# Performance work log

Hardware: AMD Instinct MI355X
Metric: run time of the kernel (lower is better)

## Reference

```python
import jax, jax.numpy as jnp
import numpy as np

EPS = 1e-5
CH = 8            # channels_per_head
HID = 4           # max(CH // reduction, 4)
SCALE = CH ** -0.5


def _layernorm(x, g, b):
    mu = jnp.mean(x, axis=-1, keepdims=True)
    var = jnp.mean(jnp.square(x - mu), axis=-1, keepdims=True)
    return (x - mu) * jax.lax.rsqrt(var + EPS) * g + b


def setup_inputs() -> dict:
    key = jax.random.key(0)
    ks = jax.random.split(key, 12)
    s = 1.0 / np.sqrt(CH)
    sh = 1.0 / np.sqrt(HID)
    return {
        "x": jax.random.normal(ks[0], (32, 4, CH, 256, 256), dtype=jnp.float32),
        "Wq": jax.random.uniform(ks[1], (CH, CH), jnp.float32, -s, s),
        "Wk": jax.random.uniform(ks[2], (CH, CH), jnp.float32, -s, s),
        "Wv": jax.random.uniform(ks[3], (CH, CH), jnp.float32, -s, s),
        "Wo": jax.random.uniform(ks[4], (CH, CH), jnp.float32, -s, s),
        "bo": jax.random.uniform(ks[5], (CH,), jnp.float32, -s, s),
        "W1": jax.random.uniform(ks[6], (HID, CH), jnp.float32, -s, s),
        "b1": jax.random.uniform(ks[7], (HID,), jnp.float32, -s, s),
        "W2": jax.random.uniform(ks[8], (CH, HID), jnp.float32, -sh, sh),
        "b2": jax.random.uniform(ks[9], (CH,), jnp.float32, -sh, sh),
        "g1": jnp.ones((CH,), jnp.float32),
        "beta1": jnp.zeros((CH,), jnp.float32),
        "g2": jnp.ones((CH,), jnp.float32),
        "beta2": jnp.zeros((CH,), jnp.float32),
        "gate": jnp.full((1,), 0.5, jnp.float32),
    }


def reference(x, Wq, Wk, Wv, Wo, bo, W1, b1, W2, b2, g1, beta1, g2, beta2, gate):
    # x: (B, n_heads, CH, H, W); pool over spatial dims -> (B, n_heads, CH)
    x_pooled = jnp.mean(x, axis=(-2, -1))
    xn = _layernorm(x_pooled, g1, beta1)
    Q = xn @ Wq.T
    K = xn @ Wk.T
    V = xn @ Wv.T
    # tiny attention across heads: scores (B, n_heads, n_heads)
    attn = jax.nn.softmax(jnp.einsum('bhc,bgc->bhg', Q, K) * SCALE, axis=-1)
    attn_out = jnp.einsum('bhg,bgc->bhc', attn, V) @ Wo.T + bo
    x_attn = x_pooled + attn_out
    xn2 = _layernorm(x_attn, g2, beta2)
    ffn = jax.nn.gelu(xn2 @ W1.T + b1, approximate=False) @ W2.T + b2
    x_out = x_attn + ffn
    g = jax.nn.sigmoid(gate)
    aw = g * (x_out - x_pooled) + x_pooled      # (B, n_heads, CH)
    return x * (1.0 + aw[..., None, None])
```

## Files before the change

### kernel.cpp

```cpp
#include <hip/hip_runtime.h>
#include <math.h>

#define CH 8
#define NH 4
#define HID 4
#define SPATIAL 65536
#define NSLICE 1024
#define NHALF  2048
#define HALF4  8192
#define EPS 1e-5f

typedef float nf4 __attribute__((ext_vector_type(4)));

__global__ __launch_bounds__(256)
void pool_kernel(const float* __restrict__ x, float* __restrict__ partial) {
    const int half = blockIdx.x;
    const nf4* xs = (const nf4*)x + (size_t)half * HALF4;
    const int tid = threadIdx.x;

    nf4 a0 = {0,0,0,0}, a1 = {0,0,0,0}, a2 = {0,0,0,0}, a3 = {0,0,0,0};
    int k = tid;
#pragma unroll
    for (int it = 0; it < 8; ++it) {
        a0 += xs[k];
        a1 += xs[k + 256];
        a2 += xs[k + 512];
        a3 += xs[k + 768];
        k += 1024;
    }
    nf4 a = (a0 + a1) + (a2 + a3);
    float sum = (a.x + a.y) + (a.z + a.w);

    for (int off = 32; off; off >>= 1) sum += __shfl_down(sum, off, 64);
    __shared__ float part[4];
    if ((tid & 63) == 0) part[tid >> 6] = sum;
    __syncthreads();
    if (tid == 0)
        partial[half] = (part[0] + part[1]) + (part[2] + part[3]);
}

__global__ __launch_bounds__(256)
void scale_fused(const float* __restrict__ x,
                 const float* __restrict__ partial,
                 const float* __restrict__ Wq, const float* __restrict__ Wk,
                 const float* __restrict__ Wv, const float* __restrict__ Wo,
                 const float* __restrict__ bo,
                 const float* __restrict__ W1, const float* __restrict__ b1,
                 const float* __restrict__ W2, const float* __restrict__ b2,
                 const float* __restrict__ g1, const float* __restrict__ beta1,
                 const float* __restrict__ g2, const float* __restrict__ beta2,
                 const float* __restrict__ gate,
                 float* __restrict__ out) {
    const int half  = blockIdx.x;
    const int slice = half >> 1;
    const int b     = slice >> 5;
    const int hh    = (slice >> 3) & 3;
    const int cc    = slice & 7;
    const int tid   = threadIdx.x;

    __shared__ float Kl[NH][CH], Vl[NH][CH], fac[NH][CH];

    float xp[CH], Q[CH];
    if (tid < NH) {
        const float* pr = partial + b * (NH * CH * 2) + tid * (CH * 2);
#pragma unroll
        for (int c = 0; c < CH; ++c)
            xp[c] = (pr[c * 2] + pr[c * 2 + 1]) * (1.0f / SPATIAL);
        float mu = 0.f;
#pragma unroll
        for (int c = 0; c < CH; ++c) mu += xp[c];
        mu *= 0.125f;
        float var = 0.f;
#pragma unroll
        for (int c = 0; c < CH; ++c) { float d = xp[c] - mu; var += d * d; }
        var *= 0.125f;
        float rs = rsqrtf(var + EPS);
        float xn[CH];
#pragma unroll
        for (int c = 0; c < CH; ++c) xn[c] = (xp[c] - mu) * rs * g1[c] + beta1[c];
#pragma unroll
        for (int c = 0; c < CH; ++c) {
            float q = 0.f, k = 0.f, v = 0.f;
#pragma unroll
            for (int j = 0; j < CH; ++j) {
                q += xn[j] * Wq[c * CH + j];
                k += xn[j] * Wk[c * CH + j];
                v += xn[j] * Wv[c * CH + j];
            }
            Q[c] = q; Kl[tid][c] = k; Vl[tid][c] = v;
        }
    }
    __syncthreads();
    if (tid < NH) {
        float sc[NH], mx = -1e30f;
#pragma unroll
        for (int g = 0; g < NH; ++g) {
            float s = 0.f;
#pragma unroll
            for (int c = 0; c < CH; ++c) s += Q[c] * Kl[g][c];
            s *= 0.35355339059327373f;
            sc[g] = s; mx = fmaxf(mx, s);
        }
        float den = 0.f;
#pragma unroll
        for (int g = 0; g < NH; ++g) { sc[g] = __expf(sc[g] - mx); den += sc[g]; }
        const float inv = 1.0f / den;
        float ao[CH];
#pragma unroll
        for (int c = 0; c < CH; ++c) {
            float a = 0.f;
#pragma unroll
            for (int g = 0; g < NH; ++g) a += sc[g] * Vl[g][c];
            ao[c] = a * inv;
        }
        float xa[CH];
#pragma unroll
        for (int c = 0; c < CH; ++c) {
            float o = bo[c];
#pragma unroll
            for (int j = 0; j < CH; ++j) o += ao[j] * Wo[c * CH + j];
            xa[c] = xp[c] + o;
        }
        float mu = 0.f;
#pragma unroll
        for (int c = 0; c < CH; ++c) mu += xa[c];
        mu *= 0.125f;
        float var = 0.f;
#pragma unroll
        for (int c = 0; c < CH; ++c) { float d = xa[c] - mu; var += d * d; }
        var *= 0.125f;
        float rs = rsqrtf(var + EPS);
        float xn2[CH];
#pragma unroll
        for (int c = 0; c < CH; ++c) xn2[c] = (xa[c] - mu) * rs * g2[c] + beta2[c];
        float h1[HID];
#pragma unroll
        for (int i = 0; i < HID; ++i) {
            float t = b1[i];
#pragma unroll
            for (int c = 0; c < CH; ++c) t += xn2[c] * W1[i * CH + c];
            h1[i] = 0.5f * t * (1.0f + erff(t * 0.70710678118654752f));
        }
        const float gs = 1.0f / (1.0f + __expf(-gate[0]));
#pragma unroll
        for (int c = 0; c < CH; ++c) {
            float f = b2[c];
#pragma unroll
            for (int i = 0; i < HID; ++i) f += h1[i] * W2[c * HID + i];
            float xo = xa[c] + f;
            fac[tid][c] = 1.0f + gs * (xo - xp[c]) + xp[c];
        }
    }
    __syncthreads();
    const float f = fac[hh][cc];

    const nf4* xs = (const nf4*)x + (size_t)half * HALF4;
    nf4*       os = (nf4*)out     + (size_t)half * HALF4;
    int k = tid;
#pragma unroll
    for (int it = 0; it < 8; ++it) {
        nf4 v0 = xs[k];
        nf4 v1 = xs[k + 256];
        nf4 v2 = xs[k + 512];
        nf4 v3 = xs[k + 768];
        v0 *= f; v1 *= f; v2 *= f; v3 *= f;
        __builtin_nontemporal_store(v0, &os[k]);
        __builtin_nontemporal_store(v1, &os[k + 256]);
        __builtin_nontemporal_store(v2, &os[k + 512]);
        __builtin_nontemporal_store(v3, &os[k + 768]);
        k += 1024;
    }
}

extern "C" void kernel_launch(void* const* d_in, const int* in_sizes, int n_in,
                              void* d_out, int out_size, void* d_ws, size_t ws_size,
                              hipStream_t stream) {
    const float* x     = (const float*)d_in[0];
    const float* Wq    = (const float*)d_in[1];
    const float* Wk    = (const float*)d_in[2];
    const float* Wv    = (const float*)d_in[3];
    const float* Wo    = (const float*)d_in[4];
    const float* bo    = (const float*)d_in[5];
    const float* W1    = (const float*)d_in[6];
    const float* b1    = (const float*)d_in[7];
    const float* W2    = (const float*)d_in[8];
    const float* b2    = (const float*)d_in[9];
    const float* g1    = (const float*)d_in[10];
    const float* beta1 = (const float*)d_in[11];
    const float* g2    = (const float*)d_in[12];
    const float* beta2 = (const float*)d_in[13];
    const float* gate  = (const float*)d_in[14];
    float* out = (float*)d_out;

    float* partial = (float*)d_ws;

    pool_kernel<<<NHALF, 256, 0, stream>>>(x, partial);
    scale_fused<<<NHALF, 256, 0, stream>>>(x, partial,
                                           Wq, Wk, Wv, Wo, bo,
                                           W1, b1, W2, b2,
                                           g1, beta1, g2, beta2,
                                           gate, out);
}
```

Measured before the change: 129.7 us.

## Fuse pooling and scaling into one cooperative kernel with grid sync

Replaces the separate pooling and scaling kernels with a single persistent cooperative kernel. Each block pools its slices, then a grid-wide barrier precedes recomputation of the tiny attention/FFN and the scaling pass. This is meant to remove the second launch and the inter-kernel gap. In exchange it adds the grid-sync cost and ties the grid size to occupancy queries.

```diff
diff --git a/kernel.cpp b/kernel.cpp
--- a/kernel.cpp
+++ b/kernel.cpp
@@ -1,5 +1,8 @@
 #include <hip/hip_runtime.h>
+#include <hip/hip_cooperative_groups.h>
 #include <math.h>
+
+namespace cg = cooperative_groups;
 
 #define CH 8
 #define NH 4
@@ -12,163 +15,170 @@
 
 typedef float nf4 __attribute__((ext_vector_type(4)));
 
-__global__ __launch_bounds__(256)
-void pool_kernel(const float* __restrict__ x, float* __restrict__ partial) {
-    const int half = blockIdx.x;
-    const nf4* xs = (const nf4*)x + (size_t)half * HALF4;
+__global__ __launch_bounds__(256, 8)
+void fused_all(const float* __restrict__ x,
+               const float* __restrict__ Wq, const float* __restrict__ Wk,
+               const float* __restrict__ Wv, const float* __restrict__ Wo,
+               const float* __restrict__ bo,
+               const float* __restrict__ W1, const float* __restrict__ b1,
+               const float* __restrict__ W2, const float* __restrict__ b2,
+               const float* __restrict__ g1, const float* __restrict__ beta1,
+               const float* __restrict__ g2, const float* __restrict__ beta2,
+               const float* __restrict__ gate,
+               float* __restrict__ out,
+               float* __restrict__ partial,
+               int hpb) {
     const int tid = threadIdx.x;
-
-    nf4 a0 = {0,0,0,0}, a1 = {0,0,0,0}, a2 = {0,0,0,0}, a3 = {0,0,0,0};
-    int k = tid;
-#pragma unroll
-    for (int it = 0; it < 8; ++it) {
-        a0 += xs[k];
-        a1 += xs[k + 256];
-        a2 += xs[k + 512];
-        a3 += xs[k + 768];
-        k += 1024;
+    const int h0  = blockIdx.x * hpb;
+
+    __shared__ float part[4];
+    __shared__ float Kl[NH][CH], Vl[NH][CH], fac[NH][CH];
+
+    for (int i = 0; i < hpb; ++i) {
+        const int half = h0 + i;
+        if (half >= NHALF) break;
+        const nf4* xs = (const nf4*)x + (size_t)half * HALF4;
+        nf4 a0 = {0,0,0,0}, a1 = {0,0,0,0}, a2 = {0,0,0,0}, a3 = {0,0,0,0};
+        int k = tid;
+#pragma unroll
+        for (int it = 0; it < 8; ++it) {
+            a0 += xs[k];
+            a1 += xs[k + 256];
+            a2 += xs[k + 512];
+            a3 += xs[k + 768];
+            k += 1024;
+        }
+        nf4 a = (a0 + a1) + (a2 + a3);
+        float sum = (a.x + a.y) + (a.z + a.w);
+        for (int off = 32; off; off >>= 1) sum += __shfl_down(sum, off, 64);
+        if ((tid & 63) == 0) part[tid >> 6] = sum;
+        __syncthreads();
+        if (tid == 0)
+            partial[half] = (part[0] + part[1]) + (part[2] + part[3]);
+        __syncthreads();
     }
-    nf4 a = (a0 + a1) + (a2 + a3);
-    float sum = (a.x + a.y) + (a.z + a.w);
-
-    for (int off = 32; off; off >>= 1) sum += __shfl_down(sum, off, 64);
-    __shared__ float part[4];
-    if ((tid & 63) == 0) part[tid >> 6] = sum;
-    __syncthreads();
-    if (tid == 0)
-        partial[half] = (part[0] + part[1]) + (part[2] + part[3]);
-}
-
-__global__ __launch_bounds__(256)
-void scale_fused(const float* __restrict__ x,
-                 const float* __restrict__ partial,
-                 const float* __restrict__ Wq, const float* __restrict__ Wk,
-                 const float* __restrict__ Wv, const float* __restrict__ Wo,
-                 const float* __restrict__ bo,
-                 const float* __restrict__ W1, const float* __restrict__ b1,
-                 const float* __restrict__ W2, const float* __restrict__ b2,
-                 const float* __restrict__ g1, const float* __restrict__ beta1,
-                 const float* __restrict__ g2, const float* __restrict__ beta2,
-                 const float* __restrict__ gate,
-                 float* __restrict__ out) {
-    const int half  = blockIdx.x;
-    const int slice = half >> 1;
-    const int b     = slice >> 5;
-    const int hh    = (slice >> 3) & 3;
-    const int cc    = slice & 7;
-    const int tid   = threadIdx.x;
-
-    __shared__ float Kl[NH][CH], Vl[NH][CH], fac[NH][CH];
-
-    float xp[CH], Q[CH];
-    if (tid < NH) {
-        const float* pr = partial + b * (NH * CH * 2) + tid * (CH * 2);
-#pragma unroll
-        for (int c = 0; c < CH; ++c)
-            xp[c] = (pr[c * 2] + pr[c * 2 + 1]) * (1.0f / SPATIAL);
-        float mu = 0.f;
-#pragma unroll
-        for (int c = 0; c < CH; ++c) mu += xp[c];
-        mu *= 0.125f;
-        float var = 0.f;
-#pragma unroll
-        for (int c = 0; c < CH; ++c) { float d = xp[c] - mu; var += d * d; }
-        var *= 0.125f;
-        float rs = rsqrtf(var + EPS);
-        float xn[CH];
-#pragma unroll
-        for (int c = 0; c < CH; ++c) xn[c] = (xp[c] - mu) * rs * g1[c] + beta1[c];
-#pragma unroll
-        for (int c = 0; c < CH; ++c) {
-            float q = 0.f, k = 0.f, v = 0.f;
-#pragma unroll
-            for (int j = 0; j < CH; ++j) {
-                q += xn[j] * Wq[c * CH + j];
-                k += xn[j] * Wk[c * CH + j];
-                v += xn[j] * Wv[c * CH + j];
-            }
-            Q[c] = q; Kl[tid][c] = k; Vl[tid][c] = v;
-        }
-    }
-    __syncthreads();
-    if (tid < NH) {
-        float sc[NH], mx = -1e30f;
-#pragma unroll
-        for (int g = 0; g < NH; ++g) {
-            float s = 0.f;
-#pragma unroll
-            for (int c = 0; c < CH; ++c) s += Q[c] * Kl[g][c];
-            s *= 0.35355339059327373f;
-            sc[g] = s; mx = fmaxf(mx, s);
-        }
-        float den = 0.f;
-#pragma unroll
-        for (int g = 0; g < NH; ++g) { sc[g] = __expf(sc[g] - mx); den += sc[g]; }
-        const float inv = 1.0f / den;
-        float ao[CH];
-#pragma unroll
-        for (int c = 0; c < CH; ++c) {
-            float a = 0.f;
-#pragma unroll
-            for (int g = 0; g < NH; ++g) a += sc[g] * Vl[g][c];
-            ao[c] = a * inv;
-        }
-        float xa[CH];
-#pragma unroll
-        for (int c = 0; c < CH; ++c) {
-            float o = bo[c];
-#pragma unroll
-            for (int j = 0; j < CH; ++j) o += ao[j] * Wo[c * CH + j];
-            xa[c] = xp[c] + o;
-        }
-        float mu = 0.f;
-#pragma unroll
-        for (int c = 0; c < CH; ++c) mu += xa[c];
-        mu *= 0.125f;
-        float var = 0.f;
-#pragma unroll
-        for (int c = 0; c < CH; ++c) { float d = xa[c] - mu; var += d * d; }
-        var *= 0.125f;
-        float rs = rsqrtf(var + EPS);
-        float xn2[CH];
-#pragma unroll
-        for (int c = 0; c < CH; ++c) xn2[c] = (xa[c] - mu) * rs * g2[c] + beta2[c];
-        float h1[HID];
-#pragma unroll
-        for (int i = 0; i < HID; ++i) {
-            float t = b1[i];
-#pragma unroll
-            for (int c = 0; c < CH; ++c) t += xn2[c] * W1[i * CH + c];
-            h1[i] = 0.5f * t * (1.0f + erff(t * 0.70710678118654752f));
-        }
-        const float gs = 1.0f / (1.0f + __expf(-gate[0]));
-#pragma unroll
-        for (int c = 0; c < CH; ++c) {
-            float f = b2[c];
-#pragma unroll
-            for (int i = 0; i < HID; ++i) f += h1[i] * W2[c * HID + i];
-            float xo = xa[c] + f;
-            fac[tid][c] = 1.0f + gs * (xo - xp[c]) + xp[c];
-        }
-    }
-    __syncthreads();
-    const float f = fac[hh][cc];
-
-    const nf4* xs = (const nf4*)x + (size_t)half * HALF4;
-    nf4*       os = (nf4*)out     + (size_t)half * HALF4;
-    int k = tid;
-#pragma unroll
-    for (int it = 0; it < 8; ++it) {
-        nf4 v0 = xs[k];
-        nf4 v1 = xs[k + 256];
-        nf4 v2 = xs[k + 512];
-        nf4 v3 = xs[k + 768];
-        v0 *= f; v1 *= f; v2 *= f; v3 *= f;
-        __builtin_nontemporal_store(v0, &os[k]);
-        __builtin_nontemporal_store(v1, &os[k + 256]);
-        __builtin_nontemporal_store(v2, &os[k + 512]);
-        __builtin_nontemporal_store(v3, &os[k + 768]);
-        k += 1024;
+
+    cg::this_grid().sync();
+
+    for (int i = 0; i < hpb; ++i) {
+        const int half = h0 + i;
+        if (half >= NHALF) break;
+        const int slice = half >> 1;
+        const int b     = slice >> 5;
+        const int hh    = (slice >> 3) & 3;
+        const int cc    = slice & 7;
+
+        float xp[CH], Q[CH];
+        if (tid < NH) {
+            const float* pr = partial + b * (NH * CH * 2) + tid * (CH * 2);
+#pragma unroll
+            for (int c = 0; c < CH; ++c)
+                xp[c] = (pr[c * 2] + pr[c * 2 + 1]) * (1.0f / SPATIAL);
+            float mu = 0.f;
+#pragma unroll
+            for (int c = 0; c < CH; ++c) mu += xp[c];
+            mu *= 0.125f;
+            float var = 0.f;
+#pragma unroll
+            for (int c = 0; c < CH; ++c) { float d = xp[c] - mu; var += d * d; }
+            var *= 0.125f;
+            float rs = rsqrtf(var + EPS);
+            float xn[CH];
+#pragma unroll
+            for (int c = 0; c < CH; ++c) xn[c] = (xp[c] - mu) * rs * g1[c] + beta1[c];
+#pragma unroll
+            for (int c = 0; c < CH; ++c) {
+                float q = 0.f, k = 0.f, v = 0.f;
+#pragma unroll
+                for (int j = 0; j < CH; ++j) {
+                    q += xn[j] * Wq[c * CH + j];
+                    k += xn[j] * Wk[c * CH + j];
+                    v += xn[j] * Wv[c * CH + j];
+                }
+                Q[c] = q; Kl[tid][c] = k; Vl[tid][c] = v;
+            }
+        }
+        __syncthreads();
+        if (tid < NH) {
+            float sc[NH], mx = -1e30f;
+#pragma unroll
+            for (int g = 0; g < NH; ++g) {
+                float s = 0.f;
+#pragma unroll
+                for (int c = 0; c < CH; ++c) s += Q[c] * Kl[g][c];
+                s *= 0.35355339059327373f;
+                sc[g] = s; mx = fmaxf(mx, s);
+            }
+            float den = 0.f;
+#pragma unroll
+            for (int g = 0; g < NH; ++g) { sc[g] = __expf(sc[g] - mx); den += sc[g]; }
+            const float inv = 1.0f / den;
+            float ao[CH];
+#pragma unroll
+            for (int c = 0; c < CH; ++c) {
+                float a = 0.f;
+#pragma unroll
+                for (int g = 0; g < NH; ++g) a += sc[g] * Vl[g][c];
+                ao[c] = a * inv;
+            }
+            float xa[CH];
+#pragma unroll
+            for (int c = 0; c < CH; ++c) {
+                float o = bo[c];
+#pragma unroll
+                for (int j = 0; j < CH; ++j) o += ao[j] * Wo[c * CH + j];
+                xa[c] = xp[c] + o;
+            }
+            float mu = 0.f;
+#pragma unroll
+            for (int c = 0; c < CH; ++c) mu += xa[c];
+            mu *= 0.125f;
+            float var = 0.f;
+#pragma unroll
+            for (int c = 0; c < CH; ++c) { float d = xa[c] - mu; var += d * d; }
+            var *= 0.125f;
+            float rs = rsqrtf(var + EPS);
+            float xn2[CH];
+#pragma unroll
+            for (int c = 0; c < CH; ++c) xn2[c] = (xa[c] - mu) * rs * g2[c] + beta2[c];
+            float h1[HID];
+#pragma unroll
+            for (int ii = 0; ii < HID; ++ii) {
+                float t = b1[ii];
+#pragma unroll
+                for (int c = 0; c < CH; ++c) t += xn2[c] * W1[ii * CH + c];
+                h1[ii] = 0.5f * t * (1.0f + erff(t * 0.70710678118654752f));
+            }
+            const float gs = 1.0f / (1.0f + __expf(-gate[0]));
+#pragma unroll
+            for (int c = 0; c < CH; ++c) {
+                float f = b2[c];
+#pragma unroll
+                for (int ii = 0; ii < HID; ++ii) f += h1[ii] * W2[c * HID + ii];
+                float xo = xa[c] + f;
+                fac[tid][c] = 1.0f + gs * (xo - xp[c]) + xp[c];
+            }
+        }
+        __syncthreads();
+        const float f = fac[hh][cc];
+
+        const nf4* xs = (const nf4*)x + (size_t)half * HALF4;
+        nf4*       os = (nf4*)out     + (size_t)half * HALF4;
+        int k = tid;
+#pragma unroll
+        for (int it = 0; it < 8; ++it) {
+            nf4 v0 = xs[k];
+            nf4 v1 = xs[k + 256];
+            nf4 v2 = xs[k + 512];
+            nf4 v3 = xs[k + 768];
+            v0 *= f; v1 *= f; v2 *= f; v3 *= f;
+            __builtin_nontemporal_store(v0, &os[k]);
+            __builtin_nontemporal_store(v1, &os[k + 256]);
+            __builtin_nontemporal_store(v2, &os[k + 512]);
+            __builtin_nontemporal_store(v3, &os[k + 768]);
+            k += 1024;
+        }
+        __syncthreads();
     }
 }
 
@@ -191,13 +201,26 @@
     const float* beta2 = (const float*)d_in[13];
     const float* gate  = (const float*)d_in[14];
     float* out = (float*)d_out;
-
     float* partial = (float*)d_ws;
 
-    pool_kernel<<<NHALF, 256, 0, stream>>>(x, partial);
-    scale_fused<<<NHALF, 256, 0, stream>>>(x, partial,
-                                           Wq, Wk, Wv, Wo, bo,
-                                           W1, b1, W2, b2,
-                                           g1, beta1, g2, beta2,
-                                           gate, out);
+    int nCU = 256, occ = 8;
+    hipDeviceProp_t prop;
+    if (hipGetDeviceProperties(&prop, 0) == hipSuccess) nCU = prop.multiProcessorCount;
+    hipOccupancyMaxActiveBlocksPerMultiprocessor(&occ, (const void*)fused_all, 256, 0);
+    int grid = nCU * occ;
+    if (grid > NHALF) grid = NHALF;
+    int hpb = (NHALF + grid - 1) / grid;
+    grid = (NHALF + hpb - 1) / hpb;
+
+    void* args[] = {
+        (void*)&x,
+        (void*)&Wq, (void*)&Wk, (void*)&Wv, (void*)&Wo, (void*)&bo,
+        (void*)&W1, (void*)&b1, (void*)&W2, (void*)&b2,
+        (void*)&g1, (void*)&beta1, (void*)&g2, (void*)&beta2,
+        (void*)&gate,
+        (void*)&out, (void*)&partial, (void*)&hpb
+    };
+    hipLaunchCooperativeKernel((const void*)fused_all,
+                               dim3(grid), dim3(256),
+                               args, 0, stream);
 }
```

Result: slower. 258.9 us (+99.6%).
